# Kernel optimization log

Hardware: AMD Instinct MI355X
Metric: run time of the kernel (lower is better)

## Reference

```python
import jax, jax.numpy as jnp
import numpy as np
import math

B, S, D, H = 8, 1024, 1024, 16
HD = D // H  # head_features = 64
SCALE = math.sqrt(HD)


def setup_inputs() -> dict:
    key = jax.random.key(0)
    k0, k1, k2, k3, k4 = jax.random.split(key, 5)
    x = jax.random.normal(k0, (B, S, D), dtype=jnp.float32)
    attn_mask = (jax.random.uniform(k1, (B, S, S)) < 0.9).astype(jnp.float32)
    w_scale = 1.0 / math.sqrt(D)  # keep unsafe exp in finite range
    Wq = jax.random.normal(k2, (D, D), dtype=jnp.float32) * w_scale
    Wk = jax.random.normal(k3, (D, D), dtype=jnp.float32) * w_scale
    Wv = jax.random.normal(k4, (D, D), dtype=jnp.float32) * w_scale
    return {"x": x, "attn_mask": attn_mask, "Wq": Wq, "Wk": Wk, "Wv": Wv}


def reference(x, attn_mask, Wq, Wk, Wv):
    b, s, _ = x.shape

    def split_heads(t):  # [b,s,D] -> [b,H,s,HD]
        return t.reshape(b, s, H, HD).transpose(0, 2, 1, 3)

    q = split_heads(x @ Wq)
    k = split_heads(x @ Wk)
    v = split_heads(x @ Wv)

    # unsafe softmax: exp without max subtraction, multiplicative mask, +1e-8 denom
    scores = jnp.einsum('bhsd,bhtd->bhst', q, k) / SCALE
    e = jnp.exp(scores) * attn_mask[:, None, :, :]
    w = e / (e.sum(axis=3, keepdims=True) + 1e-8)

    ctx = jnp.einsum('bhst,bhtd->bhsd', w, v)  # [b,H,s,HD]
    return ctx.transpose(0, 2, 1, 3).reshape(b, s, D)
```

## Files before the change

kernel.cpp:

```cpp
#include <hip/hip_runtime.h>

#define KDIM 1024

typedef _Float16 half8 __attribute__((ext_vector_type(8)));
typedef _Float16 half4 __attribute__((ext_vector_type(4)));
typedef __fp16 fp16x2 __attribute__((ext_vector_type(2)));
typedef __fp16 fp16x4 __attribute__((ext_vector_type(4)));
typedef float f32x4 __attribute__((ext_vector_type(4)));

#if defined(__has_builtin)
#if __has_builtin(__builtin_amdgcn_global_load_lds)
#define HAVE_GLDS 1
#endif
#if __has_builtin(__builtin_amdgcn_exp2f)
#define EXP2(x) __builtin_amdgcn_exp2f(x)
#endif
#if __has_builtin(__builtin_amdgcn_cvt_pkrtz)
#define HAVE_PKRTZ 1
#endif
#if __has_builtin(__builtin_amdgcn_fdot2)
#define HAVE_FDOT2 1
#endif
#endif
#ifndef EXP2
#define EXP2(x) exp2f(x)
#endif

__device__ __forceinline__ void stage16(const _Float16* g, _Float16* wave_base, int lane) {
#ifdef HAVE_GLDS
  __builtin_amdgcn_global_load_lds(
      (const __attribute__((address_space(1))) void*)g,
      (__attribute__((address_space(3))) void*)wave_base, 16, 0, 0);
#else
  *(half8*)(wave_base + lane * 8) = *(const half8*)g;
#endif
}

#define BARRIER() __builtin_amdgcn_s_barrier()

__global__ void prep_kernel(const float* __restrict__ x, const float* __restrict__ am,
                            const float* __restrict__ Wq, const float* __restrict__ Wk,
                            const float* __restrict__ Wv, _Float16* __restrict__ xb,
                            _Float16* __restrict__ Wqkvt, unsigned long long* __restrict__ bits) {
  __shared__ _Float16 tile[32][33];
  int bid = blockIdx.x;
  if (bid < 8192) {
    size_t i = ((size_t)bid * 256 + threadIdx.x) * 4;
    float4 v = *(const float4*)(x + i);
    half4 h = { (_Float16)v.x, (_Float16)v.y, (_Float16)v.z, (_Float16)v.w };
    *(half4*)(xb + i) = h;
  } else if (bid < 11264) {
    int zz = bid - 8192;
    int z = zz >> 10;
    int rem = zz & 1023;
    int bx = rem & 31, by = rem >> 5;
    const float* src = z == 0 ? Wq : (z == 1 ? Wk : Wv);
    _Float16* dst = Wqkvt + (size_t)z * KDIM * KDIM;
    float sc = (z == 0) ? 0.18033688011112042f : 1.0f;
    int tx = threadIdx.x & 31, ty = threadIdx.x >> 5;
    int c0 = bx * 32, r0 = by * 32;
#pragma unroll
    for (int i = 0; i < 4; i++) {
      int r = r0 + ty + i * 8;
      tile[tx][ty + i * 8] = (_Float16)(src[(size_t)r * KDIM + c0 + tx] * sc);
    }
    __syncthreads();
#pragma unroll
    for (int i = 0; i < 4; i++) {
      int n = c0 + ty + i * 8;
      dst[(size_t)n * KDIM + r0 + tx] = tile[ty + i * 8][tx];
    }
  } else {
    size_t i = (size_t)(bid - 11264) * 256 + threadIdx.x;
    unsigned long long b = __ballot(am[i] != 0.0f);
    if ((threadIdx.x & 63) == 0) bits[i >> 6] = b;
  }
}

__global__ __launch_bounds__(512, 4)
void gemm_kernel(const _Float16* __restrict__ A, const _Float16* __restrict__ Bt,
                 _Float16* __restrict__ Qt, _Float16* __restrict__ Kh,
                 _Float16* __restrict__ Vth) {
  __shared__ _Float16 As[2 * 8192];
  __shared__ _Float16 Bs[2 * 6144];
  int tid = threadIdx.x;
  int lane = tid & 63, w = tid >> 6;
  int la = lane & 15, qd = lane >> 4;
  int wm = w & 1, wn = w >> 1;
  int bid = blockIdx.x;
  int wg = (bid & 7) * 64 + (bid >> 3);
  int by = wg >> 4, bx = wg & 15;
  int m0 = by * 256, n0 = bx * 192;

  int srow = lane >> 2;
  int slc = ((lane & 3) ^ ((lane >> 3) & 3)) << 3;
  const _Float16* Ab = A + (size_t)m0 * KDIM;
  const _Float16* Bb = Bt + (size_t)n0 * KDIM;
  const _Float16* pAa = Ab + (size_t)(w * 16 + srow) * KDIM + slc;
  const _Float16* pAb = Ab + (size_t)(128 + w * 16 + srow) * KDIM + slc;
  const _Float16* pBa = Bb + (size_t)(w * 16 + srow) * KDIM + slc;
  const _Float16* pBb = Bb + (size_t)(128 + w * 16 + srow) * KDIM + slc;

  _Float16* ldsA0 = As + w * 512;
  _Float16* ldsA1 = As + 4096 + w * 512;
  _Float16* ldsB0 = Bs + w * 512;
  _Float16* ldsB1 = Bs + 4096 + w * 512;

  const int rc = ((qd ^ ((la >> 1) & 3)) << 3);
  const _Float16* baseA = As + (wm * 64 + la) * 32 + rc;
  const _Float16* baseB = Bs + (wn * 16 + la) * 32 + rc;

  f32x4 acc[8][3] = {};
  half8 bf[3];

#define STAGE_AB(B)                                            \
  do {                                                         \
    stage16(pAa, ldsA0 + (B) * 8192, lane);                    \
    stage16(pAb, ldsA1 + (B) * 8192, lane);                    \
    stage16(pBa, ldsB0 + (B) * 6144, lane);                    \
    if (w < 4) stage16(pBb, ldsB1 + (B) * 6144, lane);         \
    pAa += 32; pAb += 32; pBa += 32; pBb += 32;                \
  } while (0)

#define TILE(T, CUR, NXT)                                                       \
  do {                                                                          \
    if ((T) < 31) STAGE_AB(NXT);                                                \
    _Pragma("unroll") for (int nj = 0; nj < 3; ++nj)                            \
        bf[nj] = *(const half8*)(baseB + (CUR) * 6144 + nj * 2048);             \
    __builtin_amdgcn_s_setprio(1);                                              \
    _Pragma("unroll") for (int a = 0; a < 8; ++a) {                             \
      half8 afa = *(const half8*)(baseA + (CUR) * 8192 + (a >> 2) * 4096 +      \
                                  (a & 3) * 512);                               \
      _Pragma("unroll") for (int nj = 0; nj < 3; ++nj)                          \
          acc[a][nj] = __builtin_amdgcn_mfma_f32_16x16x32_f16(                  \
              afa, bf[nj], acc[a][nj], 0, 0, 0);                                \
    }                                                                           \
    __builtin_amdgcn_s_setprio(0);                                              \
    __syncthreads();                                                            \
  } while (0)

  STAGE_AB(0);
  __syncthreads();

#pragma unroll 1
  for (int tp = 0; tp < 16; ++tp) {
    TILE(2 * tp, 0, 1);
    TILE(2 * tp + 1, 1, 0);
  }

#undef TILE
#undef STAGE_AB

  int rr = lane >> 2, c4 = lane & 3;
  _Float16* ep = As + w * 1280;
#pragma unroll
  for (int mh = 0; mh < 2; ++mh) {
    int srow0 = m0 + mh * 128 + wm * 64;
    int b = srow0 >> 10, s0 = srow0 & 1023;
#pragma unroll
    for (int nj = 0; nj < 3; ++nj) {
      int colh = n0 + wn * 16 + nj * 64;
      int whichf = colh >> 10;
      int cm = colh & 1023;
      int hh = cm >> 6, d0 = cm & 63;
      if (whichf == 1) {
        _Float16* kb = Kh + (size_t)(b * 16 + hh) * 1024 * 64;
#pragma unroll
        for (int mi = 0; mi < 4; ++mi) {
          f32x4 v = acc[mh * 4 + mi][nj];
          int s = s0 + mi * 16 + qd * 4;
#pragma unroll
          for (int rg = 0; rg < 4; ++rg)
            kb[(size_t)(s + rg) * 64 + d0 + la] = (_Float16)v[rg];
        }
      } else {
        _Float16* dst = (whichf == 0) ? Qt : Vth;
#pragma unroll
        for (int mi = 0; mi < 4; ++mi) {
          f32x4 v = acc[mh * 4 + mi][nj];
          half4 hv = { (_Float16)v[0], (_Float16)v[1], (_Float16)v[2], (_Float16)v[3] };
          *(half4*)(ep + la * 72 + mi * 16 + qd * 4) = hv;
        }
        half8 o0 = *(const half8*)(ep + rr * 72 + c4 * 16);
        half8 o1 = *(const half8*)(ep + rr * 72 + c4 * 16 + 8);
        _Float16* gp = dst + ((size_t)(b * 16 + hh) * 64 + d0 + rr) * 1024 + s0 + c4 * 16;
        *(half8*)gp = o0;
        *(half8*)(gp + 8) = o1;
      }
    }
  }
}

__global__ __launch_bounds__(512, 2)
void attn_kernel(const _Float16* __restrict__ Qt, const _Float16* __restrict__ K,
                 const _Float16* __restrict__ Vt, const unsigned long long* __restrict__ mbits,
                 float* __restrict__ out) {
  __shared__ _Float16 Ks[4][2 * 64 * 32];
  __shared__ _Float16 Vs[2][2 * 64 * 40];
  int tid = threadIdx.x;
  int lane = tid & 63, w4 = tid >> 6;
  int la = lane & 15, qd = lane >> 4;
  int linear = blockIdx.x;
  int xlo = linear & 7;
  int tmp = linear >> 3;
  int qt = tmp & 3;
  int hb = (tmp >> 2) * 8 + xlo;
  int h = hb & 15, b = hb >> 4;
  const _Float16* Qp = Qt + (size_t)hb * 64 * 1024;
  const _Float16* Kp = K + (size_t)hb * 1024 * 64;
  const _Float16* Vp = Vt + (size_t)hb * 64 * 1024;
  int q0w = qt * 256 + w4 * 16;
  half8 qf[2][2];
#pragma unroll
  for (int qi = 0; qi < 2; qi++)
#pragma unroll
    for (int ks = 0; ks < 2; ks++)
#pragma unroll
      for (int j = 0; j < 8; j++)
        qf[qi][ks][j] = Qp[(size_t)(ks * 32 + qd * 8 + j) * 1024 + q0w + qi * 128 + la];
  unsigned long long mq[2][4];
#pragma unroll
  for (int qi = 0; qi < 2; qi++) {
    const ulonglong2* mp =
        (const ulonglong2*)(mbits + ((size_t)b * 1024 + q0w + qi * 128 + la) * 16 + qd * 4);
    ulonglong2 m01 = mp[0];
    ulonglong2 m23 = mp[1];
    mq[qi][0] = m01.x; mq[qi][1] = m01.y; mq[qi][2] = m23.x; mq[qi][3] = m23.y;
  }
  f32x4 acco[2][4] = {};
  float rs[2] = {0.f, 0.f};
  int kt_t = (tid & 255) >> 2;
  int kt_d = (tid >> 8) * 32 + (((tid & 3) ^ ((tid >> 2) & 3) ^ ((tid >> 4) & 3)) << 3);
  int kc8 = ((qd ^ (la & 3) ^ (la >> 2)) << 3);
  int vd = tid >> 3;
  int vt = (tid & 7) * 8;
  int vs_off = (vt >= 32 ? 2560 : 0) + vd * 40 + (vt & 31);
#if defined(HAVE_FDOT2) && defined(HAVE_PKRTZ)
  fp16x2 one2 = { (__fp16)1.0f, (__fp16)1.0f };
#endif
  {
    half8 vv0 = *(const half8*)(Vp + (size_t)vd * 1024 + vt);
    __builtin_amdgcn_sched_barrier(0);
    stage16(Kp + (size_t)kt_t * 64 + kt_d, Ks[0] + w4 * 512, lane);
    stage16(Kp + (size_t)(64 + kt_t) * 64 + kt_d, Ks[1] + w4 * 512, lane);
    *(half8*)(Vs[0] + vs_off) = vv0;
  }
  asm volatile("s_waitcnt vmcnt(1) lgkmcnt(0)" ::: "memory");
  BARRIER();
  for (int tt = 0; tt < 16; tt++) {
    const _Float16* ks_ = Ks[tt & 3];
    const _Float16* vs_ = Vs[tt & 1];
    half8 vvn;
    if (tt < 15) {
      vvn = *(const half8*)(Vp + (size_t)vd * 1024 + (tt + 1) * 64 + vt);
      __builtin_amdgcn_sched_barrier(0);
    }
    if (tt < 14)
      stage16(Kp + (size_t)((tt + 2) * 64 + kt_t) * 64 + kt_d, Ks[(tt + 2) & 3] + w4 * 512, lane);
    unsigned long long mw0 = __shfl(mq[0][tt & 3], ((tt >> 2) << 4) + la);
    unsigned long long mw1 = __shfl(mq[1][tt & 3], ((tt >> 2) << 4) + la);
    unsigned long long mq0s = mw0 >> (qd * 4);
    unsigned long long mq1s = mw1 >> (qd * 4);
#pragma unroll
    for (int tsub = 0; tsub < 4; tsub++) {
      half8 kf0 = *(const half8*)(ks_ + (tsub * 16 + la) * 32 + kc8);
      half8 kf1 = *(const half8*)(ks_ + 2048 + (tsub * 16 + la) * 32 + kc8);
      f32x4 a0 = {}, a1 = {};
      __builtin_amdgcn_s_setprio(1);
      a0 = __builtin_amdgcn_mfma_f32_16x16x32_f16(kf0, qf[0][0], a0, 0, 0, 0);
      a1 = __builtin_amdgcn_mfma_f32_16x16x32_f16(kf0, qf[1][0], a1, 0, 0, 0);
      a0 = __builtin_amdgcn_mfma_f32_16x16x32_f16(kf1, qf[0][1], a0, 0, 0, 0);
      a1 = __builtin_amdgcn_mfma_f32_16x16x32_f16(kf1, qf[1][1], a1, 0, 0, 0);
      __builtin_amdgcn_s_setprio(0);
      half4 pf[2];
#pragma unroll
      for (int qi = 0; qi < 2; qi++) {
        const f32x4& aa = qi ? a1 : a0;
        unsigned nib = (unsigned)((qi ? mq1s : mq0s) >> (tsub * 16)) & 15u;
        float e0 = (nib & 1u) ? EXP2(aa[0]) : 0.0f;
        float e1 = (nib & 2u) ? EXP2(aa[1]) : 0.0f;
        float e2 = (nib & 4u) ? EXP2(aa[2]) : 0.0f;
        float e3 = (nib & 8u) ? EXP2(aa[3]) : 0.0f;
#ifdef HAVE_PKRTZ
        fp16x2 p01 = __builtin_amdgcn_cvt_pkrtz(e0, e1);
        fp16x2 p23 = __builtin_amdgcn_cvt_pkrtz(e2, e3);
        fp16x4 pfv = __builtin_shufflevector(p01, p23, 0, 1, 2, 3);
        pf[qi] = __builtin_bit_cast(half4, pfv);
#else
        pf[qi][0] = (_Float16)e0; pf[qi][1] = (_Float16)e1;
        pf[qi][2] = (_Float16)e2; pf[qi][3] = (_Float16)e3;
#endif
#if defined(HAVE_FDOT2) && defined(HAVE_PKRTZ)
        rs[qi] = __builtin_amdgcn_fdot2(p01, one2, rs[qi], false);
        rs[qi] = __builtin_amdgcn_fdot2(p23, one2, rs[qi], false);
#else
        rs[qi] += e0 + e1 + e2 + e3;
#endif
      }
#pragma unroll
      for (int nsub = 0; nsub < 4; nsub++) {
        half4 vf = *(const half4*)(vs_ + (tsub >> 1) * 2560 + (nsub * 16 + la) * 40 +
                                   (tsub & 1) * 16 + qd * 4);
        __builtin_amdgcn_s_setprio(1);
        acco[0][nsub] = __builtin_amdgcn_mfma_f32_16x16x16f16(pf[0], vf, acco[0][nsub], 0, 0, 0);
        acco[1][nsub] = __builtin_amdgcn_mfma_f32_16x16x16f16(pf[1], vf, acco[1][nsub], 0, 0, 0);
        __builtin_amdgcn_s_setprio(0);
      }
    }
    if (tt < 15) *(half8*)(Vs[(tt + 1) & 1] + vs_off) = vvn;
    if (tt < 14) {
      asm volatile("s_waitcnt vmcnt(1) lgkmcnt(0)" ::: "memory");
      BARRIER();
    } else if (tt == 14) {
      asm volatile("s_waitcnt vmcnt(0) lgkmcnt(0)" ::: "memory");
      BARRIER();
    }
  }
  float* op = out + (size_t)b * 1024 * 1024 + (size_t)h * 64;
#pragma unroll
  for (int qi = 0; qi < 2; qi++) {
    float r0 = rs[qi];
    r0 += __shfl_xor(r0, 16);
    r0 += __shfl_xor(r0, 32);
    float inv_q = 1.0f / (r0 + 1e-8f);
#pragma unroll
    for (int rg = 0; rg < 4; rg++) {
      float inv = __shfl(inv_q, qd * 4 + rg);
      int s = q0w + qi * 128 + qd * 4 + rg;
#pragma unroll
      for (int nsub = 0; nsub < 4; nsub++)
        op[(size_t)s * 1024 + nsub * 16 + la] = acco[qi][nsub][rg] * inv;
    }
  }
}

extern "C" void kernel_launch(void* const* d_in, const int* in_sizes, int n_in,
                              void* d_out, int out_size, void* d_ws, size_t ws_size,
                              hipStream_t stream) {
  (void)in_sizes; (void)n_in; (void)out_size; (void)ws_size;
  const float* x = (const float*)d_in[0];
  const float* am = (const float*)d_in[1];
  const float* Wq = (const float*)d_in[2];
  const float* Wk = (const float*)d_in[3];
  const float* Wv = (const float*)d_in[4];
  float* out = (float*)d_out;

  char* p = (char*)d_ws;
  _Float16* xb = (_Float16*)p;    p += (size_t)8192 * 1024 * 2;
  _Float16* Wqkvt = (_Float16*)p; p += (size_t)3 * 1024 * 1024 * 2;
  _Float16* Qt = (_Float16*)p;    p += (size_t)8192 * 1024 * 2;
  _Float16* Kh = (_Float16*)p;    p += (size_t)8192 * 1024 * 2;
  _Float16* Vth = (_Float16*)p;   p += (size_t)8192 * 1024 * 2;
  unsigned long long* mb = (unsigned long long*)p;

  prep_kernel<<<44032, 256, 0, stream>>>(x, am, Wq, Wk, Wv, xb, Wqkvt, mb);
  gemm_kernel<<<dim3(512), 512, 0, stream>>>(xb, Wqkvt, Qt, Kh, Vth);
  attn_kernel<<<512, 512, 0, stream>>>(Qt, Kh, Vth, mb, out);
}
```

Before: 240.6 us.

## Process two KV tiles per barrier and apply mask via LUT multiply

```diff
diff --git a/kernel.cpp b/kernel.cpp
--- a/kernel.cpp
+++ b/kernel.cpp
@@ -196,10 +196,12 @@
                  const _Float16* __restrict__ Vt, const unsigned long long* __restrict__ mbits,
                  float* __restrict__ out) {
   __shared__ _Float16 Ks[4][2 * 64 * 32];
-  __shared__ _Float16 Vs[2][2 * 64 * 40];
+  __shared__ _Float16 Vs[4][2 * 64 * 40];
+  __shared__ _Float16 lut16[16][4];
   int tid = threadIdx.x;
   int lane = tid & 63, w4 = tid >> 6;
   int la = lane & 15, qd = lane >> 4;
+  if (tid < 64) lut16[tid >> 2][tid & 3] = (_Float16)(float)(((tid >> 2) >> (tid & 3)) & 1);
   int linear = blockIdx.x;
   int xlo = linear & 7;
   int tmp = linear >> 3;
@@ -240,23 +242,19 @@
 #endif
   {
     half8 vv0 = *(const half8*)(Vp + (size_t)vd * 1024 + vt);
+    half8 vv1 = *(const half8*)(Vp + (size_t)vd * 1024 + 64 + vt);
     __builtin_amdgcn_sched_barrier(0);
     stage16(Kp + (size_t)kt_t * 64 + kt_d, Ks[0] + w4 * 512, lane);
     stage16(Kp + (size_t)(64 + kt_t) * 64 + kt_d, Ks[1] + w4 * 512, lane);
     *(half8*)(Vs[0] + vs_off) = vv0;
-  }
-  asm volatile("s_waitcnt vmcnt(1) lgkmcnt(0)" ::: "memory");
+    *(half8*)(Vs[1] + vs_off) = vv1;
+  }
+  asm volatile("s_waitcnt vmcnt(0) lgkmcnt(0)" ::: "memory");
   BARRIER();
-  for (int tt = 0; tt < 16; tt++) {
+
+  auto compute_tile = [&](int tt) {
     const _Float16* ks_ = Ks[tt & 3];
-    const _Float16* vs_ = Vs[tt & 1];
-    half8 vvn;
-    if (tt < 15) {
-      vvn = *(const half8*)(Vp + (size_t)vd * 1024 + (tt + 1) * 64 + vt);
-      __builtin_amdgcn_sched_barrier(0);
-    }
-    if (tt < 14)
-      stage16(Kp + (size_t)((tt + 2) * 64 + kt_t) * 64 + kt_d, Ks[(tt + 2) & 3] + w4 * 512, lane);
+    const _Float16* vs_ = Vs[tt & 3];
     unsigned long long mw0 = __shfl(mq[0][tt & 3], ((tt >> 2) << 4) + la);
     unsigned long long mw1 = __shfl(mq[1][tt & 3], ((tt >> 2) << 4) + la);
     unsigned long long mq0s = mw0 >> (qd * 4);
@@ -277,23 +275,31 @@
       for (int qi = 0; qi < 2; qi++) {
         const f32x4& aa = qi ? a1 : a0;
         unsigned nib = (unsigned)((qi ? mq1s : mq0s) >> (tsub * 16)) & 15u;
+#ifdef HAVE_PKRTZ
+        float e0 = EXP2(aa[0]);
+        float e1 = EXP2(aa[1]);
+        float e2 = EXP2(aa[2]);
+        float e3 = EXP2(aa[3]);
+        fp16x4 lv = *(const fp16x4*)lut16[nib];
+        fp16x2 l01 = __builtin_shufflevector(lv, lv, 0, 1);
+        fp16x2 l23 = __builtin_shufflevector(lv, lv, 2, 3);
+        fp16x2 p01 = __builtin_amdgcn_cvt_pkrtz(e0, e1) * l01;
+        fp16x2 p23 = __builtin_amdgcn_cvt_pkrtz(e2, e3) * l23;
+        fp16x4 pfv = __builtin_shufflevector(p01, p23, 0, 1, 2, 3);
+        pf[qi] = __builtin_bit_cast(half4, pfv);
+#if defined(HAVE_FDOT2)
+        rs[qi] = __builtin_amdgcn_fdot2(p01, one2, rs[qi], false);
+        rs[qi] = __builtin_amdgcn_fdot2(p23, one2, rs[qi], false);
+#else
+        rs[qi] += (float)p01[0] + (float)p01[1] + (float)p23[0] + (float)p23[1];
+#endif
+#else
         float e0 = (nib & 1u) ? EXP2(aa[0]) : 0.0f;
         float e1 = (nib & 2u) ? EXP2(aa[1]) : 0.0f;
         float e2 = (nib & 4u) ? EXP2(aa[2]) : 0.0f;
         float e3 = (nib & 8u) ? EXP2(aa[3]) : 0.0f;
-#ifdef HAVE_PKRTZ
-        fp16x2 p01 = __builtin_amdgcn_cvt_pkrtz(e0, e1);
-        fp16x2 p23 = __builtin_amdgcn_cvt_pkrtz(e2, e3);
-        fp16x4 pfv = __builtin_shufflevector(p01, p23, 0, 1, 2, 3);
-        pf[qi] = __builtin_bit_cast(half4, pfv);
-#else
         pf[qi][0] = (_Float16)e0; pf[qi][1] = (_Float16)e1;
         pf[qi][2] = (_Float16)e2; pf[qi][3] = (_Float16)e3;
-#endif
-#if defined(HAVE_FDOT2) && defined(HAVE_PKRTZ)
-        rs[qi] = __builtin_amdgcn_fdot2(p01, one2, rs[qi], false);
-        rs[qi] = __builtin_amdgcn_fdot2(p23, one2, rs[qi], false);
-#else
         rs[qi] += e0 + e1 + e2 + e3;
 #endif
       }
@@ -307,15 +313,30 @@
         __builtin_amdgcn_s_setprio(0);
       }
     }
-    if (tt < 15) *(half8*)(Vs[(tt + 1) & 1] + vs_off) = vvn;
-    if (tt < 14) {
-      asm volatile("s_waitcnt vmcnt(1) lgkmcnt(0)" ::: "memory");
-      BARRIER();
-    } else if (tt == 14) {
+  };
+
+#pragma unroll
+  for (int u = 0; u < 8; ++u) {
+    half8 vvA, vvB;
+    if (u < 7) {
+      vvA = *(const half8*)(Vp + (size_t)vd * 1024 + (2 * u + 2) * 64 + vt);
+      vvB = *(const half8*)(Vp + (size_t)vd * 1024 + (2 * u + 3) * 64 + vt);
+      __builtin_amdgcn_sched_barrier(0);
+      stage16(Kp + (size_t)((2 * u + 2) * 64 + kt_t) * 64 + kt_d,
+              Ks[(2 * u + 2) & 3] + w4 * 512, lane);
+      stage16(Kp + (size_t)((2 * u + 3) * 64 + kt_t) * 64 + kt_d,
+              Ks[(2 * u + 3) & 3] + w4 * 512, lane);
+    }
+    compute_tile(2 * u);
+    if (u < 7) *(half8*)(Vs[(2 * u + 2) & 3] + vs_off) = vvA;
+    compute_tile(2 * u + 1);
+    if (u < 7) {
+      *(half8*)(Vs[(2 * u + 3) & 3] + vs_off) = vvB;
       asm volatile("s_waitcnt vmcnt(0) lgkmcnt(0)" ::: "memory");
       BARRIER();
     }
   }
+
   float* op = out + (size_t)b * 1024 * 1024 + (size_t)h * 64;
 #pragma unroll
   for (int qi = 0; qi < 2; qi++) {
```

Result: slower. 274.9 us (+14.3%).
